# Performance work log

Hardware: AMD Instinct MI355X
Metric: run time of the kernel (lower is better)

## Reference

```python
import jax, jax.numpy as jnp
import numpy as np

N_NODES = 50000
N_EDGES = 800000
IN_CH = 128
HID = 256
HEADS = 4
NEG_SLOPE = 0.2


def setup_inputs() -> dict:
    key = jax.random.key(0)
    ks = jax.random.split(key, 12)
    C1 = HID // HEADS  # 64 per head, layer 1
    inp = {
        "x": jax.random.normal(ks[0], (N_NODES, IN_CH), dtype=jnp.float32),
        "edge_index": jax.random.randint(ks[1], (2, N_EDGES), 0, N_NODES, dtype=jnp.int32),
        # layer 1: GATConv(128 -> 64, heads=4, concat=True)
        "W1": jax.random.normal(ks[2], (IN_CH, HEADS * C1), dtype=jnp.float32) * (1.0 / np.sqrt(IN_CH)),
        "a_src1": jax.random.normal(ks[3], (HEADS, C1), dtype=jnp.float32) * 0.1,
        "a_dst1": jax.random.normal(ks[4], (HEADS, C1), dtype=jnp.float32) * 0.1,
        "b1": jnp.zeros((HEADS * C1,), dtype=jnp.float32),
        # layer 2: GATConv(256 -> 256, heads=1, concat=False)
        "W2": jax.random.normal(ks[5], (HID, HID), dtype=jnp.float32) * (1.0 / np.sqrt(HID)),
        "a_src2": jax.random.normal(ks[6], (1, HID), dtype=jnp.float32) * 0.1,
        "a_dst2": jax.random.normal(ks[7], (1, HID), dtype=jnp.float32) * 0.1,
        "b2": jnp.zeros((HID,), dtype=jnp.float32),
    }
    return inp


def _gat_conv(x, src, dst, W, a_src, a_dst, H, C, n_nodes):
    """One PyG-style GATConv (eval mode, self-loops already appended)."""
    h = (x @ W).reshape(n_nodes, H, C)                      # [N,H,C]
    alpha_src = jnp.sum(h * a_src[None], axis=-1)           # [N,H]
    alpha_dst = jnp.sum(h * a_dst[None], axis=-1)           # [N,H]
    e = jax.nn.leaky_relu(alpha_src[src] + alpha_dst[dst], NEG_SLOPE)  # [E,H]
    # segment softmax over incoming edges of each dst node
    m = jax.ops.segment_max(e, dst, num_segments=n_nodes)  # [N,H]
    e = jnp.exp(e - m[dst])
    denom = jax.ops.segment_sum(e, dst, num_segments=n_nodes)
    alpha = e / (denom[dst] + 1e-16)                        # [E,H]
    msg = h[src] * alpha[:, :, None]                        # [E,H,C]
    return jax.ops.segment_sum(msg, dst, num_segments=n_nodes)  # [N,H,C]


def reference(x, edge_index, W1, a_src1, a_dst1, b1, W2, a_src2, a_dst2, b2):
    n = x.shape[0]
    loops = jnp.arange(n, dtype=edge_index.dtype)
    src = jnp.concatenate([edge_index[0], loops])
    dst = jnp.concatenate([edge_index[1], loops])
    C1 = HID // HEADS
    # layer 1: heads=4, concat -> [N, HID], then ELU (dropout inactive at eval)
    h1 = _gat_conv(x, src, dst, W1, a_src1, a_dst1, HEADS, C1, n)
    h1 = jax.nn.elu(h1.reshape(n, HEADS * C1) + b1)
    # layer 2: heads=1, concat=False -> mean over heads (trivial for H=1)
    h2 = _gat_conv(h1, src, dst, W2, a_src2, a_dst2, 1, HID, n)
    return h2.reshape(n, HID) + b2
```

## Files before the change

kernel.cpp:

```cpp
#include <hip/hip_runtime.h>
#include <hip/hip_fp16.h>

#define NNODES 50000
#define NEDGES 800000
#define HIDDIM 256
#define EN (NEDGES + NNODES)
#define NTILES ((NNODES + 63)/64)
#define NT64 (NTILES*64)
#define NPART 8
#define CNT_BLOCKS (NPART*120)
#define WPREP_BLOCKS 385
#define SCANA_BLOCKS 25

constexpr float NEG = 0.2f;

typedef __attribute__((ext_vector_type(8))) short short8_t;
typedef __attribute__((ext_vector_type(4))) float floatx4;

__device__ __forceinline__ float lrelu(float v){ return v >= 0.f ? v : NEG*v; }

__device__ __forceinline__ unsigned short bf16_rn(float x){
  unsigned u = __float_as_uint(x);
  return (unsigned short)((u + 0x7FFFu + ((u >> 16) & 1u)) >> 16);
}

__device__ __forceinline__ float4 ldh4(const __half* p){
  union { float2 f; __half2 h[2]; } u;
  u.f = *reinterpret_cast<const float2*>(p);
  const float2 lo = __half22float2(u.h[0]);
  const float2 hi = __half22float2(u.h[1]);
  return make_float4(lo.x, lo.y, hi.x, hi.y);
}

__global__ __launch_bounds__(256) void k_pre1(
    const int* __restrict__ ei, int* counts, int E, int n,
    const float* __restrict__ W1, const float* __restrict__ aS1, const float* __restrict__ aD1,
    const float* __restrict__ W2, const float* __restrict__ aS2, const float* __restrict__ aD2,
    unsigned short* __restrict__ W1hi, unsigned short* __restrict__ W1lo,
    unsigned short* __restrict__ W2hi, unsigned short* __restrict__ W2lo,
    float* __restrict__ va1, float* __restrict__ va2)
{
  const int t = threadIdx.x;
  if (blockIdx.x < CNT_BLOCKS){
    const int part = blockIdx.x & (NPART-1);
    const int nchunk = CNT_BLOCKS >> 3;
    const int chunk = blockIdx.x >> 3;
    const int per = n / NPART;
    const int dlo = part*per, dhi = dlo + per;
    for (int e = chunk*256 + t; e < E; e += nchunk*256){
      const int d = ei[E + e];
      if (d >= dlo && d < dhi) atomicAdd(&counts[d], 1);
    }
    return;
  }
  const int b = blockIdx.x - CNT_BLOCKS;
  if (b < 384){
    const float* W = (b < 128) ? W1 : W2;
    unsigned short* hi = (b < 128) ? W1hi : W2hi;
    unsigned short* lo = (b < 128) ? W1lo : W2lo;
    const int idx = ((b < 128) ? b : (b - 128))*256 + t;
    const int k = idx / HIDDIM, nn = idx % HIDDIM;
    const float w = W[idx];
    const unsigned short h = bf16_rn(w);
    const unsigned short l = bf16_rn(w - __uint_as_float((unsigned)h << 16));
    const int p = ((k >> 3)*HIDDIM + nn)*8 + (k & 7);
    hi[p] = h; lo[p] = l;
  } else {
    if (t < 128){
      #pragma unroll
      for (int h = 0; h < 4; ++h){
        float s = 0.f, d = 0.f;
        for (int k = 0; k < 64; ++k){
          const float w = W1[t*HIDDIM + h*64 + k];
          s = fmaf(w, aS1[h*64 + k], s);
          d = fmaf(w, aD1[h*64 + k], d);
        }
        va1[t*8 + h] = s;
        va1[t*8 + 4 + h] = d;
      }
    } else {
      for (int c = t - 128; c < 256; c += 128){
        float s = 0.f, d = 0.f;
        for (int j = 0; j < 256; ++j){
          const float w = W2[c*HIDDIM + j];
          s = fmaf(w, aS2[j], s);
          d = fmaf(w, aD2[j], d);
        }
        va2[c*2] = s; va2[c*2+1] = d;
      }
    }
  }
}

#define SCAN_CHUNK 2048
__global__ __launch_bounds__(256) void k_pre2(
    const int* __restrict__ counts, int* __restrict__ bsum, int n,
    const float* __restrict__ X, const float* __restrict__ va1,
    __half* __restrict__ xh, float* __restrict__ as1, float* __restrict__ ad1)
{
  const int t = threadIdx.x;
  if (blockIdx.x < SCANA_BLOCKS){
    __shared__ int ws[4];
    const int idx0 = blockIdx.x*SCAN_CHUNK + t*8;
    int s = 0;
    #pragma unroll
    for (int i = 0; i < 8; ++i) if (idx0 + i < n) s += counts[idx0 + i] + 1;
    for (int off = 32; off; off >>= 1) s += __shfl_xor(s, off);
    if ((t & 63) == 0) ws[t >> 6] = s;
    __syncthreads();
    if (t == 0) bsum[blockIdx.x] = ws[0] + ws[1] + ws[2] + ws[3];
    return;
  }
  const int lane = t & 63;
  const int node = (blockIdx.x - SCANA_BLOCKS)*4 + (t >> 6);
  if (node >= n) return;
  const float2 xv = *reinterpret_cast<const float2*>(X + (size_t)node*128 + 2*lane);
  *reinterpret_cast<__half2*>(xh + (size_t)node*128 + 2*lane) = __float22half2_rn(xv);

  const float4 vs0 = *reinterpret_cast<const float4*>(va1 + (2*lane)*8);
  const float4 vd0 = *reinterpret_cast<const float4*>(va1 + (2*lane)*8 + 4);
  const float4 vs1 = *reinterpret_cast<const float4*>(va1 + (2*lane+1)*8);
  const float4 vd1 = *reinterpret_cast<const float4*>(va1 + (2*lane+1)*8 + 4);
  float ps[4], pd[4];
  ps[0] = xv.x*vs0.x + xv.y*vs1.x;  pd[0] = xv.x*vd0.x + xv.y*vd1.x;
  ps[1] = xv.x*vs0.y + xv.y*vs1.y;  pd[1] = xv.x*vd0.y + xv.y*vd1.y;
  ps[2] = xv.x*vs0.z + xv.y*vs1.z;  pd[2] = xv.x*vd0.z + xv.y*vd1.z;
  ps[3] = xv.x*vs0.w + xv.y*vs1.w;  pd[3] = xv.x*vd0.w + xv.y*vd1.w;
  #pragma unroll
  for (int h = 0; h < 4; ++h)
    for (int off = 32; off; off >>= 1){
      ps[h] += __shfl_xor(ps[h], off);
      pd[h] += __shfl_xor(pd[h], off);
    }
  if (lane == 0){
    *reinterpret_cast<float4*>(as1 + (size_t)node*4) = make_float4(ps[0],ps[1],ps[2],ps[3]);
    *reinterpret_cast<float4*>(ad1 + (size_t)node*4) = make_float4(pd[0],pd[1],pd[2],pd[3]);
  }
}

__global__ void k_scan_b(const int* __restrict__ bsum, int* __restrict__ boff,
                         int* __restrict__ offs, int nb, int n){
  if (threadIdx.x == 0){
    int run = 0;
    for (int i = 0; i < nb; ++i){ boff[i] = run; run += bsum[i]; }
    offs[n] = run;
  }
}
__global__ __launch_bounds__(256) void k_scan_c(const int* __restrict__ counts,
                                                const int* __restrict__ boff,
                                                int* __restrict__ offs,
                                                int* __restrict__ cursor, int n){
  __shared__ int sc[256];
  const int t = threadIdx.x;
  const int idx0 = blockIdx.x*SCAN_CHUNK + t*8;
  int v[8], pre[8], s = 0;
  #pragma unroll
  for (int i = 0; i < 8; ++i){
    v[i] = (idx0 + i < n) ? counts[idx0 + i] + 1 : 0;
    pre[i] = s; s += v[i];
  }
  sc[t] = s;
  __syncthreads();
  int run = s;
  for (int off = 1; off < 256; off <<= 1){
    int add = (t >= off) ? sc[t - off] : 0;
    __syncthreads();
    sc[t] += add;
    __syncthreads();
  }
  const int excl = sc[t] - run;
  const int toff = boff[blockIdx.x] + excl;
  #pragma unroll
  for (int i = 0; i < 8; ++i){
    if (idx0 + i < n){
      const int o = toff + pre[i];
      offs[idx0 + i] = o;
      cursor[idx0 + i] = o;
    }
  }
}

__global__ __launch_bounds__(256) void k_scatter(const int* __restrict__ ei, int* cursor,
                          int* __restrict__ esrc, int E, int n){
  const int part = blockIdx.x & (NPART-1);
  const int nchunk = gridDim.x >> 3;
  const int chunk = blockIdx.x >> 3;
  const int per = n / NPART;
  const int dlo = part*per, dhi = dlo + per;
  const int total = E + n;
  for (int e = chunk*256 + threadIdx.x; e < total; e += nchunk*256){
    const int d = (e < E) ? ei[E + e] : (e - E);
    if (d >= dlo && d < dhi){
      const int s = (e < E) ? ei[e] : d;
      esrc[atomicAdd(&cursor[d], 1)] = s;
    }
  }
}

__global__ __launch_bounds__(256) void k_prep4(
    const float* __restrict__ as_, const float* __restrict__ ad_,
    const int* __restrict__ offs, const int* __restrict__ esrc,
    __half* __restrict__ p16, float* __restrict__ rdinv, int n)
{
  constexpr float SHIFT = 2.0f;
  const int l4 = threadIdx.x & 15;
  const int node = blockIdx.x*16 + (threadIdx.x >> 4);
  if (node >= n) return;
  const int start = offs[node], end = offs[node+1];

  const float4 adv4 = *reinterpret_cast<const float4*>(ad_ + (size_t)node*4);
  const float adv[4] = {adv4.x, adv4.y, adv4.z, adv4.w};
  float dsum[4] = {0.f, 0.f, 0.f, 0.f};

  for (int e = start + l4; e < end; e += 16){
    const int s = esrc[e];
    const float4 av = *reinterpret_cast<const float4*>(as_ + (size_t)s*4);
    const float a[4] = {av.x, av.y, av.z, av.w};
    union { float2 f; __half2 h2[2]; } o;
    float wq[4];
    #pragma unroll
    for (int h = 0; h < 4; ++h){
      const __half w16 = __float2half(__expf(lrelu(a[h] + adv[h]) - SHIFT));
      wq[h] = __half2float(w16);
      dsum[h] += wq[h];
    }
    o.h2[0] = __half2{__float2half(wq[0]), __float2half(wq[1])};
    o.h2[1] = __half2{__float2half(wq[2]), __float2half(wq[3])};
    *reinterpret_cast<float2*>(&p16[(size_t)4*e]) = o.f;
  }
  #pragma unroll
  for (int h = 0; h < 4; ++h)
    for (int off = 8; off; off >>= 1) dsum[h] += __shfl_xor(dsum[h], off);

  if (l4 == 0){
    *reinterpret_cast<float4*>(rdinv + (size_t)node*4) =
      make_float4(1.f/(dsum[0]+1e-16f), 1.f/(dsum[1]+1e-16f),
                  1.f/(dsum[2]+1e-16f), 1.f/(dsum[3]+1e-16f));
  }
}

__global__ __launch_bounds__(256) void k_agg1(
    const __half* __restrict__ xh, const __half* __restrict__ p16,
    const int* __restrict__ offs, const int* __restrict__ esrc,
    const float* __restrict__ rdinv, unsigned short* __restrict__ xagg, int n)
{
  const int l2 = threadIdx.x & 31;
  const int node = blockIdx.x*8 + (threadIdx.x >> 5);
  if (node >= n) return;
  const int start = offs[node], end = offs[node+1];
  const __half* hp = xh + 4*l2;

  float acc[4][4] = {};
  int e = start;
  for (; e + 8 <= end; e += 8){
    int s[8]; float2 pv[8]; float2 xv[8];
    #pragma unroll
    for (int i = 0; i < 8; ++i) s[i] = esrc[e+i];
    #pragma unroll
    for (int i = 0; i < 8; ++i) pv[i] = *reinterpret_cast<const float2*>(p16 + (size_t)4*(e+i));
    #pragma unroll
    for (int i = 0; i < 8; ++i) xv[i] = *reinterpret_cast<const float2*>(hp + (size_t)s[i]*128);
    #pragma unroll
    for (int i = 0; i < 8; ++i){
      union { float2 f; __half2 h2[2]; } ux; ux.f = xv[i];
      const float2 x01 = __half22float2(ux.h2[0]);
      const float2 x23 = __half22float2(ux.h2[1]);
      union { float2 f; __half2 h2[2]; } up; up.f = pv[i];
      const float2 p01 = __half22float2(up.h2[0]);
      const float2 p23 = __half22float2(up.h2[1]);
      const float ph[4] = {p01.x, p01.y, p23.x, p23.y};
      const float xc[4] = {x01.x, x01.y, x23.x, x23.y};
      #pragma unroll
      for (int h = 0; h < 4; ++h)
        #pragma unroll
        for (int c = 0; c < 4; ++c)
          acc[h][c] = fmaf(ph[h], xc[c], acc[h][c]);
    }
  }
  for (; e < end; ++e){
    const int s = esrc[e];
    union { float2 f; __half2 h2[2]; } ux;
    ux.f = *reinterpret_cast<const float2*>(hp + (size_t)s*128);
    const float2 x01 = __half22float2(ux.h2[0]);
    const float2 x23 = __half22float2(ux.h2[1]);
    union { float2 f; __half2 h2[2]; } up;
    up.f = *reinterpret_cast<const float2*>(p16 + (size_t)4*e);
    const float2 p01 = __half22float2(up.h2[0]);
    const float2 p23 = __half22float2(up.h2[1]);
    const float ph[4] = {p01.x, p01.y, p23.x, p23.y};
    const float xc[4] = {x01.x, x01.y, x23.x, x23.y};
    #pragma unroll
    for (int h = 0; h < 4; ++h)
      #pragma unroll
      for (int c = 0; c < 4; ++c)
        acc[h][c] = fmaf(ph[h], xc[c], acc[h][c]);
  }
  const float4 rv = *reinterpret_cast<const float4*>(rdinv + (size_t)node*4);
  const float rd[4] = {rv.x, rv.y, rv.z, rv.w};
  #pragma unroll
  for (int h = 0; h < 4; ++h){
    uint2 pk;
    pk.x = (unsigned)bf16_rn(acc[h][0]*rd[h]) | ((unsigned)bf16_rn(acc[h][1]*rd[h]) << 16);
    pk.y = (unsigned)bf16_rn(acc[h][2]*rd[h]) | ((unsigned)bf16_rn(acc[h][3]*rd[h]) << 16);
    *reinterpret_cast<uint2*>(xagg + (size_t)node*512 + h*128 + 4*l2) = pk;
  }
}

__global__ __launch_bounds__(256) void k_gemm1(
    const unsigned short* __restrict__ Xagg,
    const unsigned short* __restrict__ Bhi, const unsigned short* __restrict__ Blo,
    const float* __restrict__ b1, const float* __restrict__ va2,
    __half* __restrict__ h1e, float* __restrict__ as2, float* __restrict__ ad2, int M)
{
  __shared__ float lred_s[64][4], lred_d[64][4];
  const int tid = threadIdx.x;
  const int w = tid >> 6, l = tid & 63;
  const int lr = l & 15, lg = l >> 4;
  const int row0 = blockIdx.x*64;
  const int n0 = w*64;
  floatx4 acc[4][4] = {};

  for (int ks = 0; ks < 4; ++ks){
    short8_t a_[4], bh[4], bl[4];
    #pragma unroll
    for (int m = 0; m < 4; ++m){
      const size_t ao = (size_t)(row0 + 16*m + lr)*512 + w*128 + ks*32 + lg*8;
      a_[m] = *reinterpret_cast<const short8_t*>(&Xagg[ao]);
    }
    #pragma unroll
    for (int n = 0; n < 4; ++n){
      const int boff = (((ks*4 + lg)*HIDDIM) + n0 + 16*n + lr)*8;
      bh[n] = *reinterpret_cast<const short8_t*>(&Bhi[boff]);
      bl[n] = *reinterpret_cast<const short8_t*>(&Blo[boff]);
    }
    #pragma unroll
    for (int m = 0; m < 4; ++m)
      #pragma unroll
      for (int n = 0; n < 4; ++n){
        acc[m][n] = __builtin_amdgcn_mfma_f32_16x16x32_bf16(a_[m], bh[n], acc[m][n], 0,0,0);
        acc[m][n] = __builtin_amdgcn_mfma_f32_16x16x32_bf16(a_[m], bl[n], acc[m][n], 0,0,0);
      }
  }

  float bcol[4], v2s[4], v2d[4];
  #pragma unroll
  for (int n = 0; n < 4; ++n){
    const int col = n0 + 16*n + lr;
    bcol[n] = b1[col];
    v2s[n] = va2[col*2];
    v2d[n] = va2[col*2+1];
  }
  #pragma unroll
  for (int m = 0; m < 4; ++m){
    #pragma unroll
    for (int r = 0; r < 4; ++r){
      const int row = row0 + 16*m + lg*4 + r;
      float ps = 0.f, pd = 0.f;
      #pragma unroll
      for (int n = 0; n < 4; ++n){
        float v = acc[m][n][r] + bcol[n];
        v = v > 0.f ? v : __expf(v) - 1.f;
        if (row < M) h1e[(size_t)row*HIDDIM + n0 + 16*n + lr] = __float2half(v);
        ps = fmaf(v, v2s[n], ps);
        pd = fmaf(v, v2d[n], pd);
      }
      #pragma unroll
      for (int off = 1; off <= 8; off <<= 1){
        ps += __shfl_xor(ps, off);
        pd += __shfl_xor(pd, off);
      }
      const int rloc = 16*m + lg*4 + r;
      if (lr == 0){ lred_s[rloc][w] = ps; lred_d[rloc][w] = pd; }
    }
  }
  __syncthreads();
  if (tid < 64 && row0 + tid < M){
    as2[row0+tid] = lred_s[tid][0]+lred_s[tid][1]+lred_s[tid][2]+lred_s[tid][3];
    ad2[row0+tid] = lred_d[tid][0]+lred_d[tid][1]+lred_d[tid][2]+lred_d[tid][3];
  }
}

__global__ __launch_bounds__(256) void k_agg2(
    const __half* __restrict__ Hs,
    const float* __restrict__ as2, const float* __restrict__ ad2,
    const int* __restrict__ offs, const int* __restrict__ esrc,
    unsigned short* __restrict__ xagg2, int n)
{
  constexpr float SHIFT = 4.0f;
  const int lane = threadIdx.x & 63;
  const int node = blockIdx.x*4 + (threadIdx.x >> 6);
  if (node >= n) return;
  const int start = offs[node], end = offs[node+1];
  const float adn = ad2[node];
  const __half* hp = Hs + 4*lane;

  float4 a0 = {0,0,0,0}, a1 = {0,0,0,0}, a2 = {0,0,0,0}, a3 = {0,0,0,0};
  float dsum = 0.f;
  int e = start;
  for (; e + 4 <= end; e += 4){
    const int s0 = esrc[e+0], s1 = esrc[e+1], s2 = esrc[e+2], s3 = esrc[e+3];
    const float w0 = __expf(lrelu(as2[s0] + adn) - SHIFT);
    const float w1 = __expf(lrelu(as2[s1] + adn) - SHIFT);
    const float w2 = __expf(lrelu(as2[s2] + adn) - SHIFT);
    const float w3 = __expf(lrelu(as2[s3] + adn) - SHIFT);
    dsum += (w0 + w1) + (w2 + w3);
    const float4 h0 = ldh4(hp + (size_t)s0*HIDDIM);
    const float4 h1 = ldh4(hp + (size_t)s1*HIDDIM);
    const float4 h2 = ldh4(hp + (size_t)s2*HIDDIM);
    const float4 h3 = ldh4(hp + (size_t)s3*HIDDIM);
    a0.x = fmaf(w0, h0.x, a0.x); a0.y = fmaf(w0, h0.y, a0.y);
    a0.z = fmaf(w0, h0.z, a0.z); a0.w = fmaf(w0, h0.w, a0.w);
    a1.x = fmaf(w1, h1.x, a1.x); a1.y = fmaf(w1, h1.y, a1.y);
    a1.z = fmaf(w1, h1.z, a1.z); a1.w = fmaf(w1, h1.w, a1.w);
    a2.x = fmaf(w2, h2.x, a2.x); a2.y = fmaf(w2, h2.y, a2.y);
    a2.z = fmaf(w2, h2.z, a2.z); a2.w = fmaf(w2, h2.w, a2.w);
    a3.x = fmaf(w3, h3.x, a3.x); a3.y = fmaf(w3, h3.y, a3.y);
    a3.z = fmaf(w3, h3.z, a3.z); a3.w = fmaf(w3, h3.w, a3.w);
  }
  for (; e < end; ++e){
    const int s = esrc[e];
    const float w = __expf(lrelu(as2[s] + adn) - SHIFT);
    dsum += w;
    const float4 hv = ldh4(hp + (size_t)s*HIDDIM);
    a0.x = fmaf(w, hv.x, a0.x); a0.y = fmaf(w, hv.y, a0.y);
    a0.z = fmaf(w, hv.z, a0.z); a0.w = fmaf(w, hv.w, a0.w);
  }
  const float rd = 1.f/(dsum + 1e-16f);
  float4 acc;
  acc.x = ((a0.x + a1.x) + (a2.x + a3.x)) * rd;
  acc.y = ((a0.y + a1.y) + (a2.y + a3.y)) * rd;
  acc.z = ((a0.z + a1.z) + (a2.z + a3.z)) * rd;
  acc.w = ((a0.w + a1.w) + (a2.w + a3.w)) * rd;

  uint2 pk;
  pk.x = (unsigned)bf16_rn(acc.x) | ((unsigned)bf16_rn(acc.y) << 16);
  pk.y = (unsigned)bf16_rn(acc.z) | ((unsigned)bf16_rn(acc.w) << 16);
  *reinterpret_cast<uint2*>(xagg2 + (size_t)node*HIDDIM + 4*lane) = pk;
}

__global__ __launch_bounds__(256) void k_gemm2(
    const unsigned short* __restrict__ Xagg2,
    const unsigned short* __restrict__ Bhi, const unsigned short* __restrict__ Blo,
    const float* __restrict__ b2, float* __restrict__ Out, int M)
{
  const int tid = threadIdx.x;
  const int w = tid >> 6, l = tid & 63;
  const int lr = l & 15, lg = l >> 4;
  const int row0 = blockIdx.x*64;
  const int n0 = w*64;
  floatx4 acc[4][4] = {};

  for (int ks = 0; ks < 8; ++ks){
    short8_t a_[4], bh[4], bl[4];
    #pragma unroll
    for (int m = 0; m < 4; ++m){
      const size_t ao = (size_t)(row0 + 16*m + lr)*HIDDIM + ks*32 + lg*8;
      a_[m] = *reinterpret_cast<const short8_t*>(&Xagg2[ao]);
    }
    #pragma unroll
    for (int n = 0; n < 4; ++n){
      const int boff = (((ks*4 + lg)*HIDDIM) + n0 + 16*n + lr)*8;
      bh[n] = *reinterpret_cast<const short8_t*>(&Bhi[boff]);
      bl[n] = *reinterpret_cast<const short8_t*>(&Blo[boff]);
    }
    #pragma unroll
    for (int m = 0; m < 4; ++m)
      #pragma unroll
      for (int n = 0; n < 4; ++n){
        acc[m][n] = __builtin_amdgcn_mfma_f32_16x16x32_bf16(a_[m], bh[n], acc[m][n], 0,0,0);
        acc[m][n] = __builtin_amdgcn_mfma_f32_16x16x32_bf16(a_[m], bl[n], acc[m][n], 0,0,0);
      }
  }

  float bcol[4];
  #pragma unroll
  for (int n = 0; n < 4; ++n) bcol[n] = b2[n0 + 16*n + lr];
  #pragma unroll
  for (int m = 0; m < 4; ++m){
    #pragma unroll
    for (int r = 0; r < 4; ++r){
      const int row = row0 + 16*m + lg*4 + r;
      if (row < M){
        #pragma unroll
        for (int n = 0; n < 4; ++n)
          Out[(size_t)row*HIDDIM + n0 + 16*n + lr] = acc[m][n][r] + bcol[n];
      }
    }
  }
}

extern "C" void kernel_launch(void* const* d_in, const int* in_sizes, int n_in,
                              void* d_out, int out_size, void* d_ws, size_t ws_size,
                              hipStream_t stream)
{
  const float* x    = (const float*)d_in[0];
  const int*   ei   = (const int*)  d_in[1];
  const float* W1   = (const float*)d_in[2];
  const float* aS1  = (const float*)d_in[3];
  const float* aD1  = (const float*)d_in[4];
  const float* b1   = (const float*)d_in[5];
  const float* W2   = (const float*)d_in[6];
  const float* aS2  = (const float*)d_in[7];
  const float* aD2  = (const float*)d_in[8];
  const float* b2   = (const float*)d_in[9];
  float* out = (float*)d_out;

  char* ws = (char*)d_ws;
  size_t off = 0;
  auto alloc = [&](size_t bytes){ void* p = ws + off; off += (bytes + 255) & ~255ull; return p; };

  unsigned short* xagg  = (unsigned short*)alloc((size_t)NT64*512*sizeof(short));
  __half*         h1e   = (__half*)alloc((size_t)NT64*HIDDIM*sizeof(__half));
  unsigned short* xagg2 = (unsigned short*)alloc((size_t)NT64*HIDDIM*sizeof(short));
  __half*         xh    = (__half*)xagg2;
  __half* p16   = (__half*)alloc((size_t)4*EN*sizeof(__half));
  float* as1    = (float*)alloc((size_t)NNODES*4*sizeof(float));
  float* ad1    = (float*)alloc((size_t)NNODES*4*sizeof(float));
  float* rdinv1 = (float*)alloc((size_t)NNODES*4*sizeof(float));
  float* as2    = (float*)alloc((size_t)NNODES*sizeof(float));
  float* ad2    = (float*)alloc((size_t)NNODES*sizeof(float));
  float* va1    = (float*)alloc(128*8*sizeof(float));
  float* va2    = (float*)alloc(256*2*sizeof(float));
  unsigned short* W1hi = (unsigned short*)alloc((size_t)128*HIDDIM*sizeof(short));
  unsigned short* W1lo = (unsigned short*)alloc((size_t)128*HIDDIM*sizeof(short));
  unsigned short* W2hi = (unsigned short*)alloc((size_t)256*HIDDIM*sizeof(short));
  unsigned short* W2lo = (unsigned short*)alloc((size_t)256*HIDDIM*sizeof(short));
  int*   counts = (int*)alloc((size_t)NNODES*sizeof(int));
  int*   offs   = (int*)alloc((size_t)(NNODES+1)*sizeof(int));
  int*   cursor = (int*)alloc((size_t)NNODES*sizeof(int));
  int*   bsum   = (int*)alloc(64*sizeof(int));
  int*   boff   = (int*)alloc(64*sizeof(int));
  int*   esrc   = (int*)alloc((size_t)EN*sizeof(int));

  const int nscan = (NNODES + SCAN_CHUNK - 1)/SCAN_CHUNK;
  const int node_grid = (NNODES + 3)/4;

  hipMemsetAsync(counts, 0, (size_t)NNODES*sizeof(int), stream);
  k_pre1<<<CNT_BLOCKS + WPREP_BLOCKS, 256, 0, stream>>>(
      ei, counts, NEDGES, NNODES,
      W1, aS1, aD1, W2, aS2, aD2, W1hi, W1lo, W2hi, W2lo, va1, va2);
  k_pre2<<<SCANA_BLOCKS + node_grid, 256, 0, stream>>>(
      counts, bsum, NNODES, x, va1, xh, as1, ad1);
  k_scan_b    <<<1, 64, 0, stream>>>(bsum, boff, offs, nscan, NNODES);
  k_scan_c    <<<nscan, 256, 0, stream>>>(counts, boff, offs, cursor, NNODES);
  k_scatter   <<<NPART*120, 256, 0, stream>>>(ei, cursor, esrc, NEDGES, NNODES);

  k_prep4<<<(NNODES+15)/16, 256, 0, stream>>>(as1, ad1, offs, esrc, p16, rdinv1, NNODES);
  k_agg1<<<(NNODES+7)/8, 256, 0, stream>>>(xh, p16, offs, esrc, rdinv1, xagg, NNODES);
  k_gemm1<<<NTILES, 256, 0, stream>>>(xagg, W1hi, W1lo, b1, va2, h1e, as2, ad2, NNODES);

  k_agg2<<<node_grid, 256, 0, stream>>>(h1e, as2, ad2, offs, esrc, xagg2, NNODES);
  k_gemm2<<<NTILES, 256, 0, stream>>>(xagg2, W2hi, W2lo, b2, out, NNODES);
}
```

Baseline: 310.9 us.

## Fuse attention-weight prep into layer-1 aggregation via LDS and merge scan kernels

```diff
diff --git a/kernel.cpp b/kernel.cpp
--- a/kernel.cpp
+++ b/kernel.cpp
@@ -11,6 +11,7 @@
 #define CNT_BLOCKS (NPART*120)
 #define WPREP_BLOCKS 385
 #define SCANA_BLOCKS 25
+#define DEGCAP 128
 
 constexpr float NEG = 0.2f;
 
@@ -138,20 +139,23 @@
   }
 }
 
-__global__ void k_scan_b(const int* __restrict__ bsum, int* __restrict__ boff,
-                         int* __restrict__ offs, int nb, int n){
-  if (threadIdx.x == 0){
-    int run = 0;
-    for (int i = 0; i < nb; ++i){ boff[i] = run; run += bsum[i]; }
-    offs[n] = run;
-  }
-}
 __global__ __launch_bounds__(256) void k_scan_c(const int* __restrict__ counts,
-                                                const int* __restrict__ boff,
+                                                const int* __restrict__ bsum,
                                                 int* __restrict__ offs,
-                                                int* __restrict__ cursor, int n){
+                                                int* __restrict__ cursor, int n, int nb){
   __shared__ int sc[256];
+  __shared__ int base_s;
   const int t = threadIdx.x;
+  if (t == 0){
+    int bse = 0;
+    for (int i = 0; i < (int)blockIdx.x; ++i) bse += bsum[i];
+    base_s = bse;
+    if (blockIdx.x == 0){
+      int tot = 0;
+      for (int i = 0; i < nb; ++i) tot += bsum[i];
+      offs[n] = tot;
+    }
+  }
   const int idx0 = blockIdx.x*SCAN_CHUNK + t*8;
   int v[8], pre[8], s = 0;
   #pragma unroll
@@ -169,7 +173,7 @@
     __syncthreads();
   }
   const int excl = sc[t] - run;
-  const int toff = boff[blockIdx.x] + excl;
+  const int toff = base_s + excl;
   #pragma unroll
   for (int i = 0; i < 8; ++i){
     if (idx0 + i < n){
@@ -197,24 +201,32 @@
   }
 }
 
-__global__ __launch_bounds__(256) void k_prep4(
-    const float* __restrict__ as_, const float* __restrict__ ad_,
+__global__ __launch_bounds__(256) void k_agg1(
+    const __half* __restrict__ xh,
+    const float* __restrict__ as1, const float* __restrict__ ad1,
     const int* __restrict__ offs, const int* __restrict__ esrc,
-    __half* __restrict__ p16, float* __restrict__ rdinv, int n)
+    unsigned short* __restrict__ xagg, int n)
 {
   constexpr float SHIFT = 2.0f;
-  const int l4 = threadIdx.x & 15;
-  const int node = blockIdx.x*16 + (threadIdx.x >> 4);
-  if (node >= n) return;
-  const int start = offs[node], end = offs[node+1];
-
-  const float4 adv4 = *reinterpret_cast<const float4*>(ad_ + (size_t)node*4);
-  const float adv[4] = {adv4.x, adv4.y, adv4.z, adv4.w};
+  __shared__ int    sl[8][DEGCAP];
+  __shared__ float2 wl[8][DEGCAP];
+  __shared__ float  rdl[8][4];
+  const int g = threadIdx.x >> 5;
+  const int l2 = threadIdx.x & 31;
+  const int node = blockIdx.x*8 + g;
+  int start = 0, end = 0;
+  float adv[4] = {0.f, 0.f, 0.f, 0.f};
+  if (node < n){
+    start = offs[node]; end = offs[node+1];
+    const float4 adv4 = *reinterpret_cast<const float4*>(ad1 + (size_t)node*4);
+    adv[0] = adv4.x; adv[1] = adv4.y; adv[2] = adv4.z; adv[3] = adv4.w;
+  }
+  const int deg = end - start;
+
   float dsum[4] = {0.f, 0.f, 0.f, 0.f};
-
-  for (int e = start + l4; e < end; e += 16){
-    const int s = esrc[e];
-    const float4 av = *reinterpret_cast<const float4*>(as_ + (size_t)s*4);
+  for (int i = l2; i < deg; i += 32){
+    const int s = esrc[start + i];
+    const float4 av = *reinterpret_cast<const float4*>(as1 + (size_t)s*4);
     const float a[4] = {av.x, av.y, av.z, av.w};
     union { float2 f; __half2 h2[2]; } o;
     float wq[4];
@@ -224,48 +236,41 @@
       wq[h] = __half2float(w16);
       dsum[h] += wq[h];
     }
-    o.h2[0] = __half2{__float2half(wq[0]), __float2half(wq[1])};
-    o.h2[1] = __half2{__float2half(wq[2]), __float2half(wq[3])};
-    *reinterpret_cast<float2*>(&p16[(size_t)4*e]) = o.f;
+    if (i < DEGCAP){
+      o.h2[0] = __half2{__float2half(wq[0]), __float2half(wq[1])};
+      o.h2[1] = __half2{__float2half(wq[2]), __float2half(wq[3])};
+      sl[g][i] = s;
+      wl[g][i] = o.f;
+    }
   }
   #pragma unroll
   for (int h = 0; h < 4; ++h)
-    for (int off = 8; off; off >>= 1) dsum[h] += __shfl_xor(dsum[h], off);
-
-  if (l4 == 0){
-    *reinterpret_cast<float4*>(rdinv + (size_t)node*4) =
-      make_float4(1.f/(dsum[0]+1e-16f), 1.f/(dsum[1]+1e-16f),
-                  1.f/(dsum[2]+1e-16f), 1.f/(dsum[3]+1e-16f));
-  }
-}
-
-__global__ __launch_bounds__(256) void k_agg1(
-    const __half* __restrict__ xh, const __half* __restrict__ p16,
-    const int* __restrict__ offs, const int* __restrict__ esrc,
-    const float* __restrict__ rdinv, unsigned short* __restrict__ xagg, int n)
-{
-  const int l2 = threadIdx.x & 31;
-  const int node = blockIdx.x*8 + (threadIdx.x >> 5);
+    for (int off = 16; off; off >>= 1) dsum[h] += __shfl_xor(dsum[h], off);
+  if (l2 == 0){
+    #pragma unroll
+    for (int h = 0; h < 4; ++h) rdl[g][h] = 1.f/(dsum[h] + 1e-16f);
+  }
+  __syncthreads();
   if (node >= n) return;
-  const int start = offs[node], end = offs[node+1];
+
   const __half* hp = xh + 4*l2;
-
+  const int dcap = (deg < DEGCAP) ? deg : DEGCAP;
   float acc[4][4] = {};
-  int e = start;
-  for (; e + 8 <= end; e += 8){
+  int i = 0;
+  for (; i + 8 <= dcap; i += 8){
     int s[8]; float2 pv[8]; float2 xv[8];
     #pragma unroll
-    for (int i = 0; i < 8; ++i) s[i] = esrc[e+i];
-    #pragma unroll
-    for (int i = 0; i < 8; ++i) pv[i] = *reinterpret_cast<const float2*>(p16 + (size_t)4*(e+i));
-    #pragma unroll
-    for (int i = 0; i < 8; ++i) xv[i] = *reinterpret_cast<const float2*>(hp + (size_t)s[i]*128);
-    #pragma unroll
-    for (int i = 0; i < 8; ++i){
-      union { float2 f; __half2 h2[2]; } ux; ux.f = xv[i];
+    for (int j = 0; j < 8; ++j) s[j] = sl[g][i+j];
+    #pragma unroll
+    for (int j = 0; j < 8; ++j) pv[j] = wl[g][i+j];
+    #pragma unroll
+    for (int j = 0; j < 8; ++j) xv[j] = *reinterpret_cast<const float2*>(hp + (size_t)s[j]*128);
+    #pragma unroll
+    for (int j = 0; j < 8; ++j){
+      union { float2 f; __half2 h2[2]; } ux; ux.f = xv[j];
       const float2 x01 = __half22float2(ux.h2[0]);
       const float2 x23 = __half22float2(ux.h2[1]);
-      union { float2 f; __half2 h2[2]; } up; up.f = pv[i];
+      union { float2 f; __half2 h2[2]; } up; up.f = pv[j];
       const float2 p01 = __half22float2(up.h2[0]);
       const float2 p23 = __half22float2(up.h2[1]);
       const float ph[4] = {p01.x, p01.y, p23.x, p23.y};
@@ -277,14 +282,13 @@
           acc[h][c] = fmaf(ph[h], xc[c], acc[h][c]);
     }
   }
-  for (; e < end; ++e){
-    const int s = esrc[e];
+  for (; i < dcap; ++i){
+    const int s = sl[g][i];
     union { float2 f; __half2 h2[2]; } ux;
     ux.f = *reinterpret_cast<const float2*>(hp + (size_t)s*128);
     const float2 x01 = __half22float2(ux.h2[0]);
     const float2 x23 = __half22float2(ux.h2[1]);
-    union { float2 f; __half2 h2[2]; } up;
-    up.f = *reinterpret_cast<const float2*>(p16 + (size_t)4*e);
+    union { float2 f; __half2 h2[2]; } up; up.f = wl[g][i];
     const float2 p01 = __half22float2(up.h2[0]);
     const float2 p23 = __half22float2(up.h2[1]);
     const float ph[4] = {p01.x, p01.y, p23.x, p23.y};
@@ -295,13 +299,32 @@
       for (int c = 0; c < 4; ++c)
         acc[h][c] = fmaf(ph[h], xc[c], acc[h][c]);
   }
-  const float4 rv = *reinterpret_cast<const float4*>(rdinv + (size_t)node*4);
-  const float rd[4] = {rv.x, rv.y, rv.z, rv.w};
+  for (int e = start + DEGCAP; e < end; ++e){
+    const int s = esrc[e];
+    const float4 av = *reinterpret_cast<const float4*>(as1 + (size_t)s*4);
+    const float a[4] = {av.x, av.y, av.z, av.w};
+    float ph[4];
+    #pragma unroll
+    for (int h = 0; h < 4; ++h)
+      ph[h] = __expf(lrelu(a[h] + adv[h]) - SHIFT);
+    union { float2 f; __half2 h2[2]; } ux;
+    ux.f = *reinterpret_cast<const float2*>(hp + (size_t)s*128);
+    const float2 x01 = __half22float2(ux.h2[0]);
+    const float2 x23 = __half22float2(ux.h2[1]);
+    const float xc[4] = {x01.x, x01.y, x23.x, x23.y};
+    #pragma unroll
+    for (int h = 0; h < 4; ++h)
+      #pragma unroll
+      for (int c = 0; c < 4; ++c)
+        acc[h][c] = fmaf(ph[h], xc[c], acc[h][c]);
+  }
+
   #pragma unroll
   for (int h = 0; h < 4; ++h){
+    const float rd = rdl[g][h];
     uint2 pk;
-    pk.x = (unsigned)bf16_rn(acc[h][0]*rd[h]) | ((unsigned)bf16_rn(acc[h][1]*rd[h]) << 16);
-    pk.y = (unsigned)bf16_rn(acc[h][2]*rd[h]) | ((unsigned)bf16_rn(acc[h][3]*rd[h]) << 16);
+    pk.x = (unsigned)bf16_rn(acc[h][0]*rd) | ((unsigned)bf16_rn(acc[h][1]*rd) << 16);
+    pk.y = (unsigned)bf16_rn(acc[h][2]*rd) | ((unsigned)bf16_rn(acc[h][3]*rd) << 16);
     *reinterpret_cast<uint2*>(xagg + (size_t)node*512 + h*128 + 4*l2) = pk;
   }
 }
@@ -513,10 +536,8 @@
   __half*         h1e   = (__half*)alloc((size_t)NT64*HIDDIM*sizeof(__half));
   unsigned short* xagg2 = (unsigned short*)alloc((size_t)NT64*HIDDIM*sizeof(short));
   __half*         xh    = (__half*)xagg2;
-  __half* p16   = (__half*)alloc((size_t)4*EN*sizeof(__half));
   float* as1    = (float*)alloc((size_t)NNODES*4*sizeof(float));
   float* ad1    = (float*)alloc((size_t)NNODES*4*sizeof(float));
-  float* rdinv1 = (float*)alloc((size_t)NNODES*4*sizeof(float));
   float* as2    = (float*)alloc((size_t)NNODES*sizeof(float));
   float* ad2    = (float*)alloc((size_t)NNODES*sizeof(float));
   float* va1    = (float*)alloc(128*8*sizeof(float));
@@ -529,7 +550,6 @@
   int*   offs   = (int*)alloc((size_t)(NNODES+1)*sizeof(int));
   int*   cursor = (int*)alloc((size_t)NNODES*sizeof(int));
   int*   bsum   = (int*)alloc(64*sizeof(int));
-  int*   boff   = (int*)alloc(64*sizeof(int));
   int*   esrc   = (int*)alloc((size_t)EN*sizeof(int));
 
   const int nscan = (NNODES + SCAN_CHUNK - 1)/SCAN_CHUNK;
@@ -541,12 +561,10 @@
       W1, aS1, aD1, W2, aS2, aD2, W1hi, W1lo, W2hi, W2lo, va1, va2);
   k_pre2<<<SCANA_BLOCKS + node_grid, 256, 0, stream>>>(
       counts, bsum, NNODES, x, va1, xh, as1, ad1);
-  k_scan_b    <<<1, 64, 0, stream>>>(bsum, boff, offs, nscan, NNODES);
-  k_scan_c    <<<nscan, 256, 0, stream>>>(counts, boff, offs, cursor, NNODES);
+  k_scan_c    <<<nscan, 256, 0, stream>>>(counts, bsum, offs, cursor, NNODES, nscan);
   k_scatter   <<<NPART*120, 256, 0, stream>>>(ei, cursor, esrc, NEDGES, NNODES);
 
-  k_prep4<<<(NNODES+15)/16, 256, 0, stream>>>(as1, ad1, offs, esrc, p16, rdinv1, NNODES);
-  k_agg1<<<(NNODES+7)/8, 256, 0, stream>>>(xh, p16, offs, esrc, rdinv1, xagg, NNODES);
+  k_agg1<<<(NNODES+7)/8, 256, 0, stream>>>(xh, as1, ad1, offs, esrc, xagg, NNODES);
   k_gemm1<<<NTILES, 256, 0, stream>>>(xagg, W1hi, W1lo, b1, va2, h1e, as2, ad2, NNODES);
 
   k_agg2<<<node_grid, 256, 0, stream>>>(h1e, as2, ad2, offs, esrc, xagg2, NNODES);
```

Result: faster. 290.2 us (-6.7%).
